# Kernel tuning notes

Hardware: AMD Instinct MI355X
Metric: run time of the kernel (lower is better)

Reference implementation:

```python
import jax, jax.numpy as jnp
import numpy as np

BATCH, NUM_MASKS, IN_DIM, OUT_DIM = 512, 16, 1024, 1024


def setup_inputs() -> dict:
    key = jax.random.key(0)
    k1, k2, k3 = jax.random.split(key, 3)
    x = jax.random.normal(k1, (BATCH, NUM_MASKS, IN_DIM), dtype=jnp.float32)
    kernel = jax.random.normal(k2, (IN_DIM, OUT_DIM), dtype=jnp.float32) * (1.0 / np.sqrt(IN_DIM))
    masks = jax.random.uniform(k3, (NUM_MASKS, IN_DIM, OUT_DIM), dtype=jnp.float32)
    return {"x": x, "kernel": kernel, "masks": masks}


def reference(x, kernel, masks):
    # masked_kernel[m, i, o] = kernel[i, o] * masks[m, i, o]
    masked_kernel = kernel[None, :, :] * masks  # (M, I, O)
    # Original tf.scan serializes batch; equivalent math is one batched einsum:
    # out[b, m, o] = sum_i x[b, m, i] * masked_kernel[m, i, o]
    # NOTE: the executed tf.scan path applies NO activation, so neither do we.
    out = jnp.einsum('bmi,mio->bmo', x, masked_kernel)  # (B, M, O)
    return out
```

## Files before the change

### kernel.cpp

```cpp
#include <hip/hip_runtime.h>
#include <hip/hip_bf16.h>


#define BATCH 512
#define NMASK 16
#define IN_D  1024
#define OUT_D 1024

#define BM 128
#define BN 128
#define BK 64
#define NT (IN_D / BK)
#define TILE_ELEMS (BN * BK)
#define THREADS 512

using bf16x8 = __attribute__((ext_vector_type(8))) __bf16;
using bf16x4 = __attribute__((ext_vector_type(4))) __bf16;
using f32x4  = __attribute__((ext_vector_type(4))) float;
using f32x2  = __attribute__((ext_vector_type(2))) float;
using u16x4  = __attribute__((ext_vector_type(4))) unsigned short;

typedef const __attribute__((address_space(1))) void gvoid_t;
typedef __attribute__((address_space(3))) void lvoid_t;

__device__ __forceinline__ void dma16(const void* g, const void* l) {
    __builtin_amdgcn_global_load_lds((gvoid_t*)(uintptr_t)g,
                                     (lvoid_t*)(uintptr_t)l, 16, 0, 0);
}

__global__ void __launch_bounds__(THREADS, 4)
mdl_prep_w(const float* __restrict__ Kn,
           const float* __restrict__ Mk,
           unsigned short* __restrict__ Wt)
{
    const int t = threadIdx.x;
    const int l = t & 63;
    const int w = t >> 6;

    const int raw = blockIdx.x;
    const int wg  = (raw & 7) * 256 + (raw >> 3);
    const int m   = wg >> 7;
    const int ob  = (wg >> 4) & 7;
    const int k2  = wg & 15;

    const int i0 = k2 * 64 + w * 8;
    const int o0 = ob * BN + 2 * l;

    const float* mkb = Mk + ((size_t)m * IN_D + i0) * OUT_D + o0;
    const float* knb = Kn + (size_t)i0 * OUT_D + o0;

    f32x2 a[8], b[8];
#pragma unroll
    for (int r = 0; r < 8; ++r) {
        a[r] = *(const f32x2*)(mkb + (size_t)r * OUT_D);
        b[r] = *(const f32x2*)(knb + (size_t)r * OUT_D);
    }
    bf16x8 g0, g1;
#pragma unroll
    for (int r = 0; r < 8; ++r) {
        g0[r] = (__bf16)(a[r][0] * b[r][0]);
        g1[r] = (__bf16)(a[r][1] * b[r][1]);
    }
    unsigned short* dst = Wt + (size_t)wg * TILE_ELEMS + t * 16;
    *(bf16x8*)(dst)     = g0;
    *(bf16x8*)(dst + 8) = g1;
}

__global__ void __launch_bounds__(THREADS, 4)
mdl_gemm(const float* __restrict__ X,
         const unsigned short* __restrict__ Wt,
         float* __restrict__ Out)
{
    __shared__ __align__(16) unsigned short As[2][TILE_ELEMS];
    __shared__ __align__(16) unsigned short Bs[3][TILE_ELEMS];

    const int t = threadIdx.x;
    const int l = t & 63;
    const int w = t >> 6;

    const int raw = blockIdx.x;
    const int wg  = (raw & 7) * 64 + (raw >> 3);
    const int m   = wg >> 5;
    const int ob  = (wg >> 2) & 7;
    const int bb  = wg & 3;

    const int wr = w >> 2, wc = w & 3;

    f32x4 acc[4][2];
#pragma unroll
    for (int mi = 0; mi < 4; ++mi)
#pragma unroll
        for (int ni = 0; ni < 2; ++ni)
            acc[mi][ni] = (f32x4){0.f, 0.f, 0.f, 0.f};

    const int a_row = t >> 2;
    const int a_g0  = (t & 3) * 2;
    const float* Xa = X + ((size_t)(bb * BM + a_row) * NMASK + m) * IN_D + (t & 3) * 16;

    const unsigned short* Wb = Wt + (size_t)(m * 8 + ob) * NT * TILE_ELEMS;

    auto DMAB = [&](int tile, int c) {
#pragma unroll
        for (int j = 0; j < 2; ++j) {
            const unsigned short* src =
                Wb + (size_t)tile * TILE_ELEMS + (size_t)(j * 512 + w * 64 + l) * 8;
            dma16(src, &Bs[c][j * 4096 + w * 512]);
        }
    };

    f32x4 xv0, xv1, xv2, xv3;

    auto LOADX = [&](int kt) {
        xv0 = *(const f32x4*)(Xa + kt);
        xv1 = *(const f32x4*)(Xa + kt + 4);
        xv2 = *(const f32x4*)(Xa + kt + 8);
        xv3 = *(const f32x4*)(Xa + kt + 12);
    };
    auto STORE_A = [&](int buf) {
        bf16x8 v0, v1;
#pragma unroll
        for (int j = 0; j < 4; ++j) {
            v0[j] = (__bf16)xv0[j]; v0[4 + j] = (__bf16)xv1[j];
            v1[j] = (__bf16)xv2[j]; v1[4 + j] = (__bf16)xv3[j];
        }
        unsigned short* p = &As[buf][a_g0 * 1024 + a_row * 8];
        *(bf16x8*)p          = v0;
        *(bf16x8*)(p + 1024) = v1;
    };
    auto MFMAP = [&](int abuf, int bc) {
#pragma unroll
        for (int s = 0; s < 2; ++s) {
            const int gs = s * 4 + (l >> 4);
            bf16x8 bfv[2];
#pragma unroll
            for (int ni = 0; ni < 2; ++ni)
                bfv[ni] = *(const bf16x8*)
                    &Bs[bc][gs * 1024 + (wc * 32 + ni * 16 + (l & 15)) * 8];
#pragma unroll
            for (int mi = 0; mi < 4; ++mi) {
                bf16x8 af = *(const bf16x8*)
                    &As[abuf][gs * 1024 + (wr * 64 + mi * 16 + (l & 15)) * 8];
#pragma unroll
                for (int ni = 0; ni < 2; ++ni)
                    acc[mi][ni] = __builtin_amdgcn_mfma_f32_16x16x32_bf16(
                        af, bfv[ni], acc[mi][ni], 0, 0, 0);
            }
        }
    };

    LOADX(0);
    __builtin_amdgcn_sched_barrier(0);
    DMAB(0, 0);
    DMAB(1, 1);
    __builtin_amdgcn_sched_barrier(0);
    STORE_A(0);
    asm volatile("s_waitcnt lgkmcnt(0)" ::: "memory");
    __builtin_amdgcn_sched_barrier(0);
    asm volatile("s_waitcnt vmcnt(2)" ::: "memory");
    __builtin_amdgcn_sched_barrier(0);
    __builtin_amdgcn_s_barrier();
    __builtin_amdgcn_sched_barrier(0);

    int c_cur = 0, c_nxt = 1, c_far = 2;

    for (int tt = 0; tt < NT; ++tt) {
        if (tt + 1 < NT) {
            LOADX((tt + 1) * BK);
            __builtin_amdgcn_sched_barrier(0);
        }
        DMAB((tt + 2 < NT) ? tt + 2 : 0, c_far);
        __builtin_amdgcn_sched_barrier(0);

        __builtin_amdgcn_s_setprio(1);
        MFMAP(tt & 1, c_cur);
        __builtin_amdgcn_s_setprio(0);

        if (tt + 1 < NT) STORE_A((tt + 1) & 1);

        asm volatile("s_waitcnt lgkmcnt(0)" ::: "memory");
        __builtin_amdgcn_sched_barrier(0);
        asm volatile("s_waitcnt vmcnt(2)" ::: "memory");
        __builtin_amdgcn_sched_barrier(0);
        __builtin_amdgcn_s_barrier();
        __builtin_amdgcn_sched_barrier(0);

        const int tmp = c_cur; c_cur = c_nxt; c_nxt = c_far; c_far = tmp;
    }
    asm volatile("s_waitcnt vmcnt(0)" ::: "memory");

    const int r0 = bb * BM + wr * 64 + (l >> 4) * 4;
    const int c0 = ob * BN + wc * 32 + (l & 15);
#pragma unroll
    for (int mi = 0; mi < 4; ++mi) {
#pragma unroll
        for (int j = 0; j < 4; ++j) {
            const size_t row = (size_t)(r0 + mi * 16 + j);
            float* op = Out + (row * NMASK + m) * OUT_D + c0;
#pragma unroll
            for (int ni = 0; ni < 2; ++ni)
                op[ni * 16] = acc[mi][ni][j];
        }
    }
}

#define FAKP 40
#define FBKP 34
#define FMFSZ (32 * BN)

__global__ void __launch_bounds__(THREADS, 4)
mdl_fused_fallback(const float* __restrict__ X,
                   const float* __restrict__ Kn,
                   const float* __restrict__ Mk,
                   float* __restrict__ Out)
{
    __shared__ __align__(16) float          Mf[3 * FMFSZ];
    __shared__ __align__(16) unsigned short As[BM * FAKP];
    __shared__ __align__(16) unsigned short Bs[BN * FBKP];

    const int t = threadIdx.x;
    const int l = t & 63;
    const int w = t >> 6;

    const int raw = blockIdx.x;
    const int wg  = (raw & 7) * 64 + (raw >> 3);
    const int m   = wg >> 5;
    const int ob  = (wg >> 2) & 7;
    const int bb  = wg & 3;

    const int wr = w >> 2, wc = w & 3;

    f32x4 acc[4][2];
#pragma unroll
    for (int mi = 0; mi < 4; ++mi)
#pragma unroll
        for (int ni = 0; ni < 2; ++ni)
            acc[mi][ni] = (f32x4){0.f, 0.f, 0.f, 0.f};

    const int a_row = t >> 2;
    const int a_kh  = (t & 3) * 8;
    const int o2 = (t & 63) * 2;
    const int k4 = w * 4;

    const int obase = ob * BN;
    const float* Xa  = X + ((size_t)(bb * BM + a_row) * NMASK + m) * IN_D + a_kh;
    const float* Knb = Kn + obase + o2;
    const float* Mkm = Mk + (size_t)m * IN_D * OUT_D;

    auto DMA = [&](int tile, int c) {
        const int kt = tile * 32;
#pragma unroll
        for (int j = 0; j < 2; ++j) {
            const int k = j * 16 + w * 2 + (l >> 5);
            const float* gsrc = Mkm + (size_t)(kt + k) * OUT_D + obase + (l & 31) * 4;
            dma16(gsrc, &Mf[c * FMFSZ + j * 2048 + w * 256]);
        }
    };

    DMA(0, 0);
    DMA(1, 1);
    asm volatile("s_waitcnt vmcnt(2)" ::: "memory");
    __builtin_amdgcn_sched_barrier(0);
    __builtin_amdgcn_s_barrier();
    __builtin_amdgcn_sched_barrier(0);

    int c_cur = 0, c_nxt = 1, c_far = 2;

    for (int tt = 0; tt < 32; ++tt) {
        const int kt = tt * 32;
        f32x4 xv0 = *(const f32x4*)(Xa + kt);
        f32x4 xv1 = *(const f32x4*)(Xa + kt + 4);
        f32x2 kv[4];
#pragma unroll
        for (int r = 0; r < 4; ++r)
            kv[r] = *(const f32x2*)(Knb + (size_t)(kt + k4 + r) * OUT_D);
        __builtin_amdgcn_sched_barrier(0);
        DMA((tt + 2 < 32) ? tt + 2 : 0, c_far);
        __builtin_amdgcn_sched_barrier(0);
        {
            f32x2 mvv[4];
#pragma unroll
            for (int r = 0; r < 4; ++r)
                mvv[r] = *(const f32x2*)(&Mf[c_cur * FMFSZ + (k4 + r) * BN + o2]);
#pragma unroll
            for (int c = 0; c < 2; ++c) {
                bf16x4 v;
#pragma unroll
                for (int r = 0; r < 4; ++r)
                    v[r] = (__bf16)(kv[r][c] * mvv[r][c]);
                *(bf16x4*)(&Bs[(o2 + c) * FBKP + k4]) = v;
            }
            bf16x8 va;
#pragma unroll
            for (int j = 0; j < 4; ++j) {
                va[j] = (__bf16)xv0[j]; va[4 + j] = (__bf16)xv1[j];
            }
            *(bf16x8*)(&As[a_row * FAKP + a_kh]) = va;
        }
        asm volatile("s_waitcnt lgkmcnt(0)" ::: "memory");
        __builtin_amdgcn_sched_barrier(0);
        __builtin_amdgcn_s_barrier();
        __builtin_amdgcn_sched_barrier(0);
        {
            const int kg = (l >> 4) * 8;
            bf16x8 bfv[2];
#pragma unroll
            for (int ni = 0; ni < 2; ++ni) {
                const int n = wc * 32 + ni * 16 + (l & 15);
                bf16x4 lo = *(const bf16x4*)(&Bs[n * FBKP + kg]);
                bf16x4 hi = *(const bf16x4*)(&Bs[n * FBKP + kg + 4]);
                bf16x8 f;
                f[0] = lo[0]; f[1] = lo[1]; f[2] = lo[2]; f[3] = lo[3];
                f[4] = hi[0]; f[5] = hi[1]; f[6] = hi[2]; f[7] = hi[3];
                bfv[ni] = f;
            }
#pragma unroll
            for (int mi = 0; mi < 4; ++mi) {
                const int r = wr * 64 + mi * 16 + (l & 15);
                bf16x8 af = *(const bf16x8*)(&As[r * FAKP + kg]);
#pragma unroll
                for (int ni = 0; ni < 2; ++ni)
                    acc[mi][ni] = __builtin_amdgcn_mfma_f32_16x16x32_bf16(
                        af, bfv[ni], acc[mi][ni], 0, 0, 0);
            }
        }
        asm volatile("s_waitcnt vmcnt(2)" ::: "memory");
        __builtin_amdgcn_sched_barrier(0);
        __builtin_amdgcn_s_barrier();
        __builtin_amdgcn_sched_barrier(0);
        const int tmp = c_cur; c_cur = c_nxt; c_nxt = c_far; c_far = tmp;
    }
    asm volatile("s_waitcnt vmcnt(0)" ::: "memory");

    const int r0 = bb * BM + wr * 64 + (l >> 4) * 4;
    const int c0 = ob * BN + wc * 32 + (l & 15);
#pragma unroll
    for (int mi = 0; mi < 4; ++mi) {
#pragma unroll
        for (int j = 0; j < 4; ++j) {
            const size_t row = (size_t)(r0 + mi * 16 + j);
            float* op = Out + (row * NMASK + m) * OUT_D + c0;
#pragma unroll
            for (int ni = 0; ni < 2; ++ni)
                op[ni * 16] = acc[mi][ni][j];
        }
    }
}

extern "C" void kernel_launch(void* const* d_in, const int* in_sizes, int n_in,
                              void* d_out, int out_size, void* d_ws, size_t ws_size,
                              hipStream_t stream) {
    (void)in_sizes; (void)n_in; (void)out_size;
    const float* X  = (const float*)d_in[0];
    const float* Kn = (const float*)d_in[1];
    const float* Mk = (const float*)d_in[2];
    float* Out = (float*)d_out;

    if (ws_size >= (size_t)NMASK * IN_D * OUT_D * sizeof(unsigned short)) {
        unsigned short* Wt = (unsigned short*)d_ws;
        mdl_prep_w<<<NMASK * 8 * NT, THREADS, 0, stream>>>(Kn, Mk, Wt);
        mdl_gemm<<<(BATCH / BM) * (OUT_D / BN) * NMASK, THREADS, 0, stream>>>(X, Wt, Out);
    } else {
        mdl_fused_fallback<<<512, THREADS, 0, stream>>>(X, Kn, Mk, Out);
    }
}
```

Before: 59.45 us.

## Pre-pack X to bf16 in prep kernel; LDS-free register GEMM with 32x32 MFMA

The prep kernel now also converts X to bf16 into a fragment-friendly packed layout in the workspace, alongside the masked weights. The GEMM is rewritten to skip LDS entirely. Each wave loads its MFMA fragments straight from global memory into registers, double-buffered, and computes a 64x64 tile with 32x32x16 bf16 MFMA. This removes LDS staging, barriers and in-loop conversion. In exchange it relies on L2/cache hits, since A and B tiles are re-read from global by many waves, and it needs extra workspace for the packed X.

Result: slower. 60.89 us (+2.4%).

```diff
diff --git a/kernel.cpp b/kernel.cpp
--- a/kernel.cpp
+++ b/kernel.cpp
@@ -7,18 +7,11 @@
 #define IN_D  1024
 #define OUT_D 1024
 
-#define BM 128
-#define BN 128
-#define BK 64
-#define NT (IN_D / BK)
-#define TILE_ELEMS (BN * BK)
-#define THREADS 512
-
 using bf16x8 = __attribute__((ext_vector_type(8))) __bf16;
 using bf16x4 = __attribute__((ext_vector_type(4))) __bf16;
+using f32x16 = __attribute__((ext_vector_type(16))) float;
 using f32x4  = __attribute__((ext_vector_type(4))) float;
 using f32x2  = __attribute__((ext_vector_type(2))) float;
-using u16x4  = __attribute__((ext_vector_type(4))) unsigned short;
 
 typedef const __attribute__((address_space(1))) void gvoid_t;
 typedef __attribute__((address_space(3))) void lvoid_t;
@@ -28,194 +21,179 @@
                                      (lvoid_t*)(uintptr_t)l, 16, 0, 0);
 }
 
-__global__ void __launch_bounds__(THREADS, 4)
-mdl_prep_w(const float* __restrict__ Kn,
-           const float* __restrict__ Mk,
-           unsigned short* __restrict__ Wt)
+__global__ void __launch_bounds__(512, 4)
+mdl_prep(const float* __restrict__ X,
+         const float* __restrict__ Kn,
+         const float* __restrict__ Mk,
+         unsigned short* __restrict__ Wt,
+         unsigned short* __restrict__ Xp)
+{
+    const int t   = threadIdx.x;
+    const int bid = blockIdx.x;
+
+    if (bid < 2048) {
+        const int l = t & 63;
+        const int w = t >> 6;
+        const int wg = (bid & 7) * 256 + (bid >> 3);
+        const int m  = wg >> 7;
+        const int ob = (wg >> 4) & 7;
+        const int k2 = wg & 15;
+
+        const int i0 = k2 * 64 + w * 8;
+        const int o0 = ob * 128 + 2 * l;
+
+        const float* mkb = Mk + ((size_t)m * IN_D + i0) * OUT_D + o0;
+        const float* knb = Kn + (size_t)i0 * OUT_D + o0;
+
+        f32x2 a[8], b[8];
+#pragma unroll
+        for (int r = 0; r < 8; ++r) {
+            a[r] = *(const f32x2*)(mkb + (size_t)r * OUT_D);
+            b[r] = *(const f32x2*)(knb + (size_t)r * OUT_D);
+        }
+        bf16x8 g0, g1;
+#pragma unroll
+        for (int r = 0; r < 8; ++r) {
+            g0[r] = (__bf16)(a[r][0] * b[r][0]);
+            g1[r] = (__bf16)(a[r][1] * b[r][1]);
+        }
+        unsigned short* dst = Wt + (size_t)wg * 8192 + t * 16;
+        *(bf16x8*)(dst)     = g0;
+        *(bf16x8*)(dst + 8) = g1;
+    } else {
+        const int b2    = bid - 2048;
+        const int strip = b2 >> 2;
+        const int Gq    = b2 & 3;
+        const int m  = strip >> 3;
+        const int bt = strip & 7;
+        const int row = t >> 3;
+        const int oc  = t & 7;
+
+        const float* src = X + ((size_t)(bt * 64 + row) * NMASK + m) * IN_D
+                             + Gq * 256 + oc * 32;
+        f32x4 av[8];
+#pragma unroll
+        for (int q = 0; q < 8; ++q)
+            av[q] = *(const f32x4*)(src + q * 4);
+
+        unsigned short* dstS = Xp + (size_t)strip * 65536
+                                  + (size_t)(Gq * 32 + oc * 4) * 512 + row * 8;
+#pragma unroll
+        for (int j = 0; j < 4; ++j) {
+            bf16x8 g;
+#pragma unroll
+            for (int e = 0; e < 4; ++e) {
+                g[e]     = (__bf16)av[2 * j][e];
+                g[4 + e] = (__bf16)av[2 * j + 1][e];
+            }
+            *(bf16x8*)(dstS + (size_t)j * 512) = g;
+        }
+    }
+}
+
+struct Frags { bf16x8 a[2][2]; bf16x8 b[2][2]; };
+
+__global__ void __launch_bounds__(256, 2)
+mdl_gemm2(const unsigned short* __restrict__ Xp,
+          const unsigned short* __restrict__ Wt,
+          float* __restrict__ Out)
 {
     const int t = threadIdx.x;
     const int l = t & 63;
     const int w = t >> 6;
 
     const int raw = blockIdx.x;
-    const int wg  = (raw & 7) * 256 + (raw >> 3);
-    const int m   = wg >> 7;
-    const int ob  = (wg >> 4) & 7;
-    const int k2  = wg & 15;
-
-    const int i0 = k2 * 64 + w * 8;
-    const int o0 = ob * BN + 2 * l;
-
-    const float* mkb = Mk + ((size_t)m * IN_D + i0) * OUT_D + o0;
-    const float* knb = Kn + (size_t)i0 * OUT_D + o0;
-
-    f32x2 a[8], b[8];
-#pragma unroll
-    for (int r = 0; r < 8; ++r) {
-        a[r] = *(const f32x2*)(mkb + (size_t)r * OUT_D);
-        b[r] = *(const f32x2*)(knb + (size_t)r * OUT_D);
-    }
-    bf16x8 g0, g1;
-#pragma unroll
-    for (int r = 0; r < 8; ++r) {
-        g0[r] = (__bf16)(a[r][0] * b[r][0]);
-        g1[r] = (__bf16)(a[r][1] * b[r][1]);
-    }
-    unsigned short* dst = Wt + (size_t)wg * TILE_ELEMS + t * 16;
-    *(bf16x8*)(dst)     = g0;
-    *(bf16x8*)(dst + 8) = g1;
-}
-
-__global__ void __launch_bounds__(THREADS, 4)
-mdl_gemm(const float* __restrict__ X,
-         const unsigned short* __restrict__ Wt,
-         float* __restrict__ Out)
-{
-    __shared__ __align__(16) unsigned short As[2][TILE_ELEMS];
-    __shared__ __align__(16) unsigned short Bs[3][TILE_ELEMS];
-
-    const int t = threadIdx.x;
-    const int l = t & 63;
-    const int w = t >> 6;
-
-    const int raw = blockIdx.x;
     const int wg  = (raw & 7) * 64 + (raw >> 3);
-    const int m   = wg >> 5;
-    const int ob  = (wg >> 2) & 7;
-    const int bb  = wg & 3;
-
-    const int wr = w >> 2, wc = w & 3;
-
-    f32x4 acc[4][2];
-#pragma unroll
-    for (int mi = 0; mi < 4; ++mi)
-#pragma unroll
-        for (int ni = 0; ni < 2; ++ni)
-            acc[mi][ni] = (f32x4){0.f, 0.f, 0.f, 0.f};
-
-    const int a_row = t >> 2;
-    const int a_g0  = (t & 3) * 2;
-    const float* Xa = X + ((size_t)(bb * BM + a_row) * NMASK + m) * IN_D + (t & 3) * 16;
-
-    const unsigned short* Wb = Wt + (size_t)(m * 8 + ob) * NT * TILE_ELEMS;
-
-    auto DMAB = [&](int tile, int c) {
-#pragma unroll
-        for (int j = 0; j < 2; ++j) {
-            const unsigned short* src =
-                Wb + (size_t)tile * TILE_ELEMS + (size_t)(j * 512 + w * 64 + l) * 8;
-            dma16(src, &Bs[c][j * 4096 + w * 512]);
+    const int v   = wg * 4 + w;
+    const int m   = v >> 7;
+    const int v7  = v & 127;
+    const int bt  = v7 >> 4;
+    const int ot  = v7 & 15;
+
+    const unsigned short* Ap = Xp + (size_t)(m * 8 + bt) * 65536;
+    const unsigned short* Bp = Wt + (size_t)(m * 8 + (ot >> 1)) * 131072
+                                  + (size_t)((ot & 1) * 64) * 8;
+
+    const int la = (l & 31) * 8;
+    const int ls = l >> 5;
+
+    f32x16 acc[2][2];
+#pragma unroll
+    for (int ti = 0; ti < 2; ++ti)
+#pragma unroll
+        for (int tj = 0; tj < 2; ++tj)
+#pragma unroll
+            for (int e = 0; e < 16; ++e)
+                acc[ti][tj][e] = 0.f;
+
+    auto LOADF = [&](Frags& F, int kb) {
+#pragma unroll
+        for (int s = 0; s < 2; ++s) {
+            const int G = (kb >> 3) + s * 2 + ls;
+            const unsigned short* ab = Ap + (size_t)G * 512 + la;
+            F.a[s][0] = *(const bf16x8*)(ab);
+            F.a[s][1] = *(const bf16x8*)(ab + 256);
+            const unsigned short* bb = Bp + (size_t)(G >> 3) * 8192
+                                          + (size_t)(G & 7) * 1024 + la;
+            F.b[s][0] = *(const bf16x8*)(bb);
+            F.b[s][1] = *(const bf16x8*)(bb + 256);
         }
     };
-
-    f32x4 xv0, xv1, xv2, xv3;
-
-    auto LOADX = [&](int kt) {
-        xv0 = *(const f32x4*)(Xa + kt);
-        xv1 = *(const f32x4*)(Xa + kt + 4);
-        xv2 = *(const f32x4*)(Xa + kt + 8);
-        xv3 = *(const f32x4*)(Xa + kt + 12);
+    auto MF = [&](Frags& F) {
+#pragma unroll
+        for (int s = 0; s < 2; ++s)
+#pragma unroll
+            for (int ti = 0; ti < 2; ++ti)
+#pragma unroll
+                for (int tj = 0; tj < 2; ++tj)
+                    acc[ti][tj] = __builtin_amdgcn_mfma_f32_32x32x16_bf16(
+                        F.a[s][ti], F.b[s][tj], acc[ti][tj], 0, 0, 0);
     };
-    auto STORE_A = [&](int buf) {
-        bf16x8 v0, v1;
-#pragma unroll
-        for (int j = 0; j < 4; ++j) {
-            v0[j] = (__bf16)xv0[j]; v0[4 + j] = (__bf16)xv1[j];
-            v1[j] = (__bf16)xv2[j]; v1[4 + j] = (__bf16)xv3[j];
-        }
-        unsigned short* p = &As[buf][a_g0 * 1024 + a_row * 8];
-        *(bf16x8*)p          = v0;
-        *(bf16x8*)(p + 1024) = v1;
-    };
-    auto MFMAP = [&](int abuf, int bc) {
-#pragma unroll
-        for (int s = 0; s < 2; ++s) {
-            const int gs = s * 4 + (l >> 4);
-            bf16x8 bfv[2];
-#pragma unroll
-            for (int ni = 0; ni < 2; ++ni)
-                bfv[ni] = *(const bf16x8*)
-                    &Bs[bc][gs * 1024 + (wc * 32 + ni * 16 + (l & 15)) * 8];
-#pragma unroll
-            for (int mi = 0; mi < 4; ++mi) {
-                bf16x8 af = *(const bf16x8*)
-                    &As[abuf][gs * 1024 + (wr * 64 + mi * 16 + (l & 15)) * 8];
-#pragma unroll
-                for (int ni = 0; ni < 2; ++ni)
-                    acc[mi][ni] = __builtin_amdgcn_mfma_f32_16x16x32_bf16(
-                        af, bfv[ni], acc[mi][ni], 0, 0, 0);
-            }
-        }
-    };
-
-    LOADX(0);
-    __builtin_amdgcn_sched_barrier(0);
-    DMAB(0, 0);
-    DMAB(1, 1);
-    __builtin_amdgcn_sched_barrier(0);
-    STORE_A(0);
-    asm volatile("s_waitcnt lgkmcnt(0)" ::: "memory");
-    __builtin_amdgcn_sched_barrier(0);
-    asm volatile("s_waitcnt vmcnt(2)" ::: "memory");
-    __builtin_amdgcn_sched_barrier(0);
-    __builtin_amdgcn_s_barrier();
-    __builtin_amdgcn_sched_barrier(0);
-
-    int c_cur = 0, c_nxt = 1, c_far = 2;
-
-    for (int tt = 0; tt < NT; ++tt) {
-        if (tt + 1 < NT) {
-            LOADX((tt + 1) * BK);
-            __builtin_amdgcn_sched_barrier(0);
-        }
-        DMAB((tt + 2 < NT) ? tt + 2 : 0, c_far);
-        __builtin_amdgcn_sched_barrier(0);
-
-        __builtin_amdgcn_s_setprio(1);
-        MFMAP(tt & 1, c_cur);
-        __builtin_amdgcn_s_setprio(0);
-
-        if (tt + 1 < NT) STORE_A((tt + 1) & 1);
-
-        asm volatile("s_waitcnt lgkmcnt(0)" ::: "memory");
-        __builtin_amdgcn_sched_barrier(0);
-        asm volatile("s_waitcnt vmcnt(2)" ::: "memory");
-        __builtin_amdgcn_sched_barrier(0);
-        __builtin_amdgcn_s_barrier();
-        __builtin_amdgcn_sched_barrier(0);
-
-        const int tmp = c_cur; c_cur = c_nxt; c_nxt = c_far; c_far = tmp;
-    }
-    asm volatile("s_waitcnt vmcnt(0)" ::: "memory");
-
-    const int r0 = bb * BM + wr * 64 + (l >> 4) * 4;
-    const int c0 = ob * BN + wc * 32 + (l & 15);
-#pragma unroll
-    for (int mi = 0; mi < 4; ++mi) {
-#pragma unroll
-        for (int j = 0; j < 4; ++j) {
-            const size_t row = (size_t)(r0 + mi * 16 + j);
-            float* op = Out + (row * NMASK + m) * OUT_D + c0;
-#pragma unroll
-            for (int ni = 0; ni < 2; ++ni)
-                op[ni * 16] = acc[mi][ni][j];
+
+    Frags S0, S1;
+    LOADF(S0, 0);
+    for (int kb = 0; kb < IN_D; kb += 64) {
+        LOADF(S1, kb + 32);
+        __builtin_amdgcn_sched_barrier(0);
+        MF(S0);
+        LOADF(S0, (kb + 64) & (IN_D - 1));
+        __builtin_amdgcn_sched_barrier(0);
+        MF(S1);
+    }
+
+    const int r0 = bt * 64 + 4 * ls;
+    const int c0 = ot * 64 + (l & 31);
+#pragma unroll
+    for (int ti = 0; ti < 2; ++ti) {
+#pragma unroll
+        for (int tj = 0; tj < 2; ++tj) {
+#pragma unroll
+            for (int g = 0; g < 4; ++g) {
+#pragma unroll
+                for (int q = 0; q < 4; ++q) {
+                    const int row = r0 + ti * 32 + g * 8 + q;
+                    const int col = c0 + tj * 32;
+                    Out[((size_t)row * NMASK + m) * OUT_D + col] =
+                        acc[ti][tj][g * 4 + q];
+                }
+            }
         }
     }
 }
 
 #define FAKP 40
 #define FBKP 34
-#define FMFSZ (32 * BN)
-
-__global__ void __launch_bounds__(THREADS, 4)
+#define FMFSZ (32 * 128)
+
+__global__ void __launch_bounds__(512, 4)
 mdl_fused_fallback(const float* __restrict__ X,
                    const float* __restrict__ Kn,
                    const float* __restrict__ Mk,
                    float* __restrict__ Out)
 {
     __shared__ __align__(16) float          Mf[3 * FMFSZ];
-    __shared__ __align__(16) unsigned short As[BM * FAKP];
-    __shared__ __align__(16) unsigned short Bs[BN * FBKP];
+    __shared__ __align__(16) unsigned short As[128 * FAKP];
+    __shared__ __align__(16) unsigned short Bs[128 * FBKP];
 
     const int t = threadIdx.x;
     const int l = t & 63;
@@ -241,8 +219,8 @@
     const int o2 = (t & 63) * 2;
     const int k4 = w * 4;
 
-    const int obase = ob * BN;
-    const float* Xa  = X + ((size_t)(bb * BM + a_row) * NMASK + m) * IN_D + a_kh;
+    const int obase = ob * 128;
+    const float* Xa  = X + ((size_t)(bb * 128 + a_row) * NMASK + m) * IN_D + a_kh;
     const float* Knb = Kn + obase + o2;
     const float* Mkm = Mk + (size_t)m * IN_D * OUT_D;
 
@@ -280,14 +258,14 @@
             f32x2 mvv[4];
 #pragma unroll
             for (int r = 0; r < 4; ++r)
-                mvv[r] = *(const f32x2*)(&Mf[c_cur * FMFSZ + (k4 + r) * BN + o2]);
+                mvv[r] = *(const f32x2*)(&Mf[c_cur * FMFSZ + (k4 + r) * 128 + o2]);
 #pragma unroll
             for (int c = 0; c < 2; ++c) {
-                bf16x4 v;
+                bf16x4 vv;
 #pragma unroll
                 for (int r = 0; r < 4; ++r)
-                    v[r] = (__bf16)(kv[r][c] * mvv[r][c]);
-                *(bf16x4*)(&Bs[(o2 + c) * FBKP + k4]) = v;
+                    vv[r] = (__bf16)(kv[r][c] * mvv[r][c]);
+                *(bf16x4*)(&Bs[(o2 + c) * FBKP + k4]) = vv;
             }
             bf16x8 va;
 #pragma unroll
@@ -331,8 +309,8 @@
     }
     asm volatile("s_waitcnt vmcnt(0)" ::: "memory");
 
-    const int r0 = bb * BM + wr * 64 + (l >> 4) * 4;
-    const int c0 = ob * BN + wc * 32 + (l & 15);
+    const int r0 = bb * 128 + wr * 64 + (l >> 4) * 4;
+    const int c0 = ob * 128 + wc * 32 + (l & 15);
 #pragma unroll
     for (int mi = 0; mi < 4; ++mi) {
 #pragma unroll
@@ -355,11 +333,15 @@
     const float* Mk = (const float*)d_in[2];
     float* Out = (float*)d_out;
 
-    if (ws_size >= (size_t)NMASK * IN_D * OUT_D * sizeof(unsigned short)) {
+    const size_t w_bytes = (size_t)NMASK * IN_D * OUT_D * sizeof(unsigned short);
+    const size_t x_bytes = (size_t)BATCH * NMASK * IN_D * sizeof(unsigned short);
+
+    if (ws_size >= w_bytes + x_bytes) {
         unsigned short* Wt = (unsigned short*)d_ws;
-        mdl_prep_w<<<NMASK * 8 * NT, THREADS, 0, stream>>>(Kn, Mk, Wt);
-        mdl_gemm<<<(BATCH / BM) * (OUT_D / BN) * NMASK, THREADS, 0, stream>>>(X, Wt, Out);
+        unsigned short* Xp = (unsigned short*)d_ws + w_bytes / 2;
+        mdl_prep<<<2560, 512, 0, stream>>>(X, Kn, Mk, Wt, Xp);
+        mdl_gemm2<<<512, 256, 0, stream>>>(Xp, Wt, Out);
     } else {
-        mdl_fused_fallback<<<512, THREADS, 0, stream>>>(X, Kn, Mk, Out);
-    }
-}
+        mdl_fused_fallback<<<512, 512, 0, stream>>>(X, Kn, Mk, Out);
+    }
+}
```
